# Performance work log

Measured on AMD Instinct MI355X. Metric: run time of the kernel, lower is better.

The kernel has to match this reference:

```python
import jax, jax.numpy as jnp
import numpy as np

EPS = 1e-5  # BatchNorm2d default eps


def _binarize_ste(x):
    """Forward: sign(x). Backward: hardtanh STE (grad 1 where |x|<=1, else 0)."""
    xc = jnp.clip(x, -1.0, 1.0)
    return xc + jax.lax.stop_gradient(jnp.sign(x) - xc)


def setup_inputs() -> dict:
    key = jax.random.key(0)
    k1, k2, k3, k4 = jax.random.split(key, 4)
    x = jax.random.normal(k1, (32, 256, 32, 32), dtype=jnp.float32)
    # BatchNorm affine params (affine=True)
    gamma = 1.0 + 0.1 * jax.random.normal(k2, (256,), dtype=jnp.float32)
    beta = 0.1 * jax.random.normal(k3, (256,), dtype=jnp.float32)
    # Conv weight, OIHW, bias=False
    W = 0.05 * jax.random.normal(k4, (256, 256, 3, 3), dtype=jnp.float32)
    return {"x": x, "gamma": gamma, "beta": beta, "W": W}


def reference(x, gamma, beta, W):
    # BatchNorm2d, training-mode batch statistics over (N, H, W) per channel
    mean = jnp.mean(x, axis=(0, 2, 3), keepdims=True)
    var = jnp.var(x, axis=(0, 2, 3), keepdims=True)
    xn = (x - mean) * jax.lax.rsqrt(var + EPS)
    xn = xn * gamma[None, :, None, None] + beta[None, :, None, None]
    # Conv2d_1w1a: binarize activations and weights (sign fwd / STE bwd), then conv
    a = _binarize_ste(xn)
    wb = _binarize_ste(W)
    out = jax.lax.conv_general_dilated(
        a, wb,
        window_strides=(1, 1),
        padding=((1, 1), (1, 1)),
        dimension_numbers=("NCHW", "OIHW", "NCHW"),
    )
    return out
```

## Files before the change

kernel.cpp:

```cpp
#include <hip/hip_runtime.h>
#include <hip/hip_bf16.h>


#define NIMG 32
#define C    256
#define K    256

typedef int v4i  __attribute__((ext_vector_type(4)));
typedef int v16i __attribute__((ext_vector_type(16)));

#define AHT_IMG 295936
#define AHT_KB  36992
#define AHT_ROW 1088

#define GL16(gp, lp) __builtin_amdgcn_global_load_lds(                        \
    (const __attribute__((address_space(1))) unsigned int*)(gp),              \
    (__attribute__((address_space(3))) unsigned int*)(lp), 16, 0, 0)


__global__ __launch_bounds__(256) void k_stats_packw(
    const float* __restrict__ x, const float* __restrict__ W,
    double2* __restrict__ partials, char* __restrict__ wfrag) {
  int bx = blockIdx.x;
  int tid = threadIdx.x;
  if (bx >= 2048) {
    int k = bx - 2048, c = tid;
    const float* src = W + ((size_t)k * 256 + c) * 9;
    char* dst = wfrag + (size_t)(c >> 4) * 4096 + k * 16 + (c & 15);
    #pragma unroll
    for (int t = 0; t < 9; ++t)
      dst[(size_t)t * 65536] = (src[t] > 0.0f) ? (char)1 : (char)-1;
    return;
  }
  int c = bx >> 3, grp = bx & 7;
  double s = 0.0, sq = 0.0;
  #pragma unroll
  for (int ni = 0; ni < 4; ++ni) {
    int n = grp * 4 + ni;
    const float* p = x + (size_t)n * (C * 1024) + (size_t)c * 1024;
    float4 v = ((const float4*)p)[tid];
    s += (double)v.x + (double)v.y + (double)v.z + (double)v.w;
    sq += (double)v.x * v.x + (double)v.y * v.y
        + (double)v.z * v.z + (double)v.w * v.w;
  }
  for (int o = 32; o > 0; o >>= 1) {
    s += __shfl_down(s, o);
    sq += __shfl_down(sq, o);
  }
  __shared__ double ls[4], lq[4];
  if ((tid & 63) == 0) { ls[tid >> 6] = s; lq[tid >> 6] = sq; }
  __syncthreads();
  if (tid == 0) {
    double2 r;
    r.x = ls[0] + ls[1] + ls[2] + ls[3];
    r.y = lq[0] + lq[1] + lq[2] + lq[3];
    partials[c * 8 + grp] = r;
  }
}

__global__ __launch_bounds__(256) void k_packa_i8(
    const float* __restrict__ x, const double2* __restrict__ partials,
    const float* __restrict__ gamma, const float* __restrict__ beta,
    char* __restrict__ aHT) {
  __shared__ float lf[32 * 257];
  __shared__ float lthr[256];
  __shared__ unsigned lfl[256];
  int y = blockIdx.x, n = blockIdx.y, tid = threadIdx.x;

  {
    double S = 0.0, Q = 0.0;
    #pragma unroll
    for (int g = 0; g < 8; ++g) {
      double2 p = partials[tid * 8 + g];
      S += p.x; Q += p.y;
    }
    const double N = 32768.0;
    double mean = S / N;
    double var = Q / N - mean * mean;
    double rs = 1.0 / sqrt(var + 1e-5);
    double gm = (double)gamma[tid];
    double bt = (double)beta[tid];
    float t;
    unsigned flip;
    if (gm == 0.0) {
      t = (bt > 0.0) ? -3.0e38f : 3.0e38f;
      flip = 0u;
    } else {
      t = (float)(mean - bt / (rs * gm));
      flip = (gm < 0.0) ? 1u : 0u;
    }
    lthr[tid] = t;
    lfl[tid] = flip;
  }

  #pragma unroll
  for (int it = 0; it < 8; ++it) {
    int c = it * 32 + (tid >> 3), q = tid & 7;
    float4 v = *(const float4*)(x + (size_t)n * 262144 + (size_t)c * 1024
                                + y * 32 + q * 4);
    lf[(q * 4 + 0) * 257 + c] = v.x;
    lf[(q * 4 + 1) * 257 + c] = v.y;
    lf[(q * 4 + 2) * 257 + c] = v.z;
    lf[(q * 4 + 3) * 257 + c] = v.w;
  }
  __syncthreads();
  int xl = tid & 31, cb = tid >> 5;
  unsigned wds[8];
  #pragma unroll
  for (int g = 0; g < 8; ++g) {
    unsigned wv = 0;
    #pragma unroll
    for (int jj = 0; jj < 4; ++jj) {
      int c = cb * 32 + g * 4 + jj;
      float v = lf[xl * 257 + c];
      unsigned bit = ((v > lthr[c]) ? 1u : 0u) ^ lfl[c];
      unsigned byte = bit ? 0x01u : 0xFFu;
      wv |= byte << (8 * jj);
    }
    wds[g] = wv;
  }
  char* dst = aHT + ((size_t)n * 8 + cb) * AHT_KB
            + (size_t)(y + 1) * AHT_ROW + (size_t)(xl + 1) * 32;
  uint4 u0, u1;
  u0.x = wds[0]; u0.y = wds[1]; u0.z = wds[2]; u0.w = wds[3];
  u1.x = wds[4]; u1.y = wds[5]; u1.z = wds[6]; u1.w = wds[7];
  *(uint4*)dst = u0;
  *((uint4*)dst + 1) = u1;

  uint4 z; z.x = 0; z.y = 0; z.z = 0; z.w = 0;
  if (xl < 2) {
    char* hz = aHT + ((size_t)n * 8 + cb) * AHT_KB
             + (size_t)(y + 1) * AHT_ROW + (size_t)(xl * 33) * 32;
    *(uint4*)hz = z;
    *((uint4*)hz + 1) = z;
  }
  if (y == 0 || y == 31) {
    int row = (y == 0) ? 0 : 33;
    for (int idx = tid; idx < 272; idx += 256) {
      int kb = idx / 34, xx = idx % 34;
      char* hz = aHT + ((size_t)n * 8 + kb) * AHT_KB
               + (size_t)row * AHT_ROW + (size_t)xx * 32;
      *(uint4*)hz = z;
      *((uint4*)hz + 1) = z;
    }
  }
}

__global__ __launch_bounds__(512) void k_conv_mfma(
    const char* __restrict__ aHT, const char* __restrict__ wfrag,
    float* __restrict__ out) {
  __shared__ char As[49152];
  int tid = threadIdx.x;
  int lane = tid & 63, w = tid >> 6;
  int nh = w & 3, mb = w >> 2;
  int bx = blockIdx.x;
  int lb = (bx & 7) * 32 + (bx >> 3);
  int n = lb >> 3, ys = lb & 7;
  int y0 = ys * 4;
  int yw = y0 + mb * 2;
  int xl = lane & 31, hi = lane >> 5;

  int sr = w >> 1, skb = w & 1;
  int sp = lane & 31, sh = lane >> 5;
  const char* aLane = aHT + (size_t)n * AHT_IMG + (size_t)skb * AHT_KB
                    + (size_t)sp * 32 + sh * 16;

  unsigned aRd = (unsigned)(mb * 4096 + hi * 512 + xl * 16);
  unsigned bRd = (unsigned)(hi * 4096 + (nh * 64 + xl) * 16);

  v16i a00 = {0}, a01 = {0}, a10 = {0}, a11 = {0};

  {
    const char* ag = aLane + (size_t)(y0 + 0 + sr) * AHT_ROW + 0;
    GL16(ag, As + w * 1024);
    const char* bg = wfrag + (size_t)(2 * w) * 1024 + lane * 16;
    GL16(bg, As + 8192 + (2 * w) * 1024);
    GL16(bg + 1024, As + 8192 + (2 * w + 1) * 1024);
  }
  __syncthreads();

  for (int p = 0; p < 36; ++p) {
    int cur = (p & 1) * 24576;
    if (p < 35) {
      int nxt = 24576 - cur;
      int pp = p + 1;
      int tt = pp >> 2;
      int kb0 = (pp & 3) * 2;
      int dy = tt / 3 - 1, dx = tt % 3 - 1;
      const char* ag = aLane + (size_t)kb0 * AHT_KB
                     + (size_t)(y0 + 1 + dy + sr) * AHT_ROW
                     + (size_t)(1 + dx) * 32;
      GL16(ag, As + nxt + w * 1024);
      const char* bg = wfrag + (size_t)pp * 16384 + (size_t)(2 * w) * 1024
                     + lane * 16;
      GL16(bg, As + nxt + 8192 + (2 * w) * 1024);
      GL16(bg + 1024, As + nxt + 8192 + (2 * w + 1) * 1024);
    }
    {
      const char* cb = As + cur;
      v4i A00 = *(const v4i*)(cb + aRd);
      v4i A01 = *(const v4i*)(cb + aRd + 1024);
      v4i A10 = *(const v4i*)(cb + aRd + 2048);
      v4i A11 = *(const v4i*)(cb + aRd + 3072);
      const char* bb = cb + 8192;
      v4i B0 = *(const v4i*)(bb + bRd);
      v4i B1 = *(const v4i*)(bb + bRd + 512);
      v4i B2 = *(const v4i*)(bb + bRd + 8192);
      v4i B3 = *(const v4i*)(bb + bRd + 8192 + 512);
      a00 = __builtin_amdgcn_mfma_i32_32x32x32_i8(A00, B0, a00, 0, 0, 0);
      a01 = __builtin_amdgcn_mfma_i32_32x32x32_i8(A00, B1, a01, 0, 0, 0);
      a10 = __builtin_amdgcn_mfma_i32_32x32x32_i8(A10, B0, a10, 0, 0, 0);
      a11 = __builtin_amdgcn_mfma_i32_32x32x32_i8(A10, B1, a11, 0, 0, 0);
      a00 = __builtin_amdgcn_mfma_i32_32x32x32_i8(A01, B2, a00, 0, 0, 0);
      a01 = __builtin_amdgcn_mfma_i32_32x32x32_i8(A01, B3, a01, 0, 0, 0);
      a10 = __builtin_amdgcn_mfma_i32_32x32x32_i8(A11, B2, a10, 0, 0, 0);
      a11 = __builtin_amdgcn_mfma_i32_32x32x32_i8(A11, B3, a11, 0, 0, 0);
    }
    __syncthreads();
  }

  size_t ob0 = (size_t)n * 262144 + (size_t)(nh * 64 + xl) * 1024
             + (size_t)yw * 32 + 4 * hi;
  #pragma unroll
  for (int r = 0; r < 2; ++r) {
    #pragma unroll
    for (int nb = 0; nb < 2; ++nb) {
      v16i av = (r == 0) ? (nb == 0 ? a00 : a01) : (nb == 0 ? a10 : a11);
      float* obp = out + ob0 + (size_t)nb * 32768 + r * 32;
      #pragma unroll
      for (int q = 0; q < 4; ++q) {
        float4 f;
        f.x = (float)av[q * 4 + 0];
        f.y = (float)av[q * 4 + 1];
        f.z = (float)av[q * 4 + 2];
        f.w = (float)av[q * 4 + 3];
        *(float4*)(obp + 8 * q) = f;
      }
    }
  }
}


__global__ __launch_bounds__(256) void k_stats_part_fb(
    const float* __restrict__ x, double2* __restrict__ partials) {
  int grp = blockIdx.x;
  int c = blockIdx.y;
  int tid = threadIdx.x;
  double s = 0.0, sq = 0.0;
  #pragma unroll
  for (int ni = 0; ni < 4; ++ni) {
    int n = grp * 4 + ni;
    const float* p = x + (size_t)n * (C * 1024) + (size_t)c * 1024;
    float4 v = ((const float4*)p)[tid];
    s += (double)v.x + (double)v.y + (double)v.z + (double)v.w;
    sq += (double)v.x * v.x + (double)v.y * v.y
        + (double)v.z * v.z + (double)v.w * v.w;
  }
  for (int o = 32; o > 0; o >>= 1) {
    s += __shfl_down(s, o);
    sq += __shfl_down(sq, o);
  }
  __shared__ double ls[4], lq[4];
  if ((tid & 63) == 0) { ls[tid >> 6] = s; lq[tid >> 6] = sq; }
  __syncthreads();
  if (tid == 0) {
    double2 r;
    r.x = ls[0] + ls[1] + ls[2] + ls[3];
    r.y = lq[0] + lq[1] + lq[2] + lq[3];
    partials[c * 8 + grp] = r;
  }
}

__global__ __launch_bounds__(256) void k_packw_corr_final(
    const float* __restrict__ W, const double2* __restrict__ partials,
    const float* __restrict__ gamma, const float* __restrict__ beta,
    unsigned* __restrict__ wp, int* __restrict__ corr,
    unsigned* __restrict__ zp, float* __restrict__ t_out,
    unsigned* __restrict__ flip_out) {
  int bk = blockIdx.x;
  int tid = threadIdx.x;
  if (bk == 256) {
    int c = tid;
    double S = 0.0, Q = 0.0;
    #pragma unroll
    for (int g = 0; g < 8; ++g) {
      double2 p = partials[c * 8 + g];
      S += p.x; Q += p.y;
    }
    const double N = 32768.0;
    double mean = S / N;
    double var = Q / N - mean * mean;
    double rs = 1.0 / sqrt(var + 1e-5);
    double g = (double)gamma[c];
    double b = (double)beta[c];
    float t;
    unsigned flip;
    if (g == 0.0) {
      t = (b > 0.0) ? -3.0e38f : 3.0e38f;
      flip = 0u;
    } else {
      t = (float)(mean - b / (rs * g));
      flip = (g < 0.0) ? 1u : 0u;
    }
    t_out[c] = t;
    flip_out[c] = flip;
    return;
  }
  int k = bk;
  __shared__ unsigned lw[72];
  float w[9];
  const float* src = W + (size_t)k * 2304 + (size_t)tid * 9;
  #pragma unroll
  for (int t = 0; t < 9; ++t) w[t] = src[t];
  int lane = tid & 63, wv = tid >> 6;
  #pragma unroll
  for (int t = 0; t < 9; ++t) {
    unsigned long long m = __ballot(w[t] > 0.0f);
    if (lane == 0) {
      lw[t * 8 + 2 * wv] = (unsigned)m;
      lw[t * 8 + 2 * wv + 1] = (unsigned)(m >> 32);
    }
  }
  __syncthreads();
  if (tid < 72) wp[(size_t)k * 72 + tid] = lw[tid];
  if (tid >= 128 && tid < 144) {
    int cls = tid - 128;
    int sum = 0;
    #pragma unroll
    for (int t = 0; t < 9; ++t) {
      int dy = t / 3 - 1, dx = t % 3 - 1;
      bool inv = (((cls & 1) && dx == -1) || ((cls & 2) && dx == 1) ||
                  ((cls & 4) && dy == -1) || ((cls & 8) && dy == 1));
      if (inv) {
        #pragma unroll
        for (int j = 0; j < 8; ++j) sum += __popc(lw[t * 8 + j]);
      }
    }
    corr[k * 16 + cls] = sum;
  }
  if (bk == 0 && tid >= 192 && tid < 200) zp[tid - 192] = 0u;
}

__global__ __launch_bounds__(256) void k_packa_bits(
    const float* __restrict__ x, const float* __restrict__ t,
    const unsigned* __restrict__ flip, unsigned* __restrict__ ap) {
  int n = blockIdx.y;
  int p0 = blockIdx.x * 64;
  int pix = threadIdx.x & 63;
  int q = threadIdx.x >> 6;
  unsigned w0 = 0, w1 = 0;
  const float* xb = x + (size_t)n * (C * 1024) + p0 + pix;
  #pragma unroll
  for (int i = 0; i < 64; ++i) {
    int c = q * 64 + i;
    float tv = t[c];
    unsigned fl = flip[c];
    float v = xb[(size_t)c * 1024];
    unsigned bit = ((v > tv) ? 1u : 0u) ^ fl;
    if (i < 32) w0 |= bit << i;
    else        w1 |= bit << (i - 32);
  }
  uint2 st; st.x = w0; st.y = w1;
  *(uint2*)(ap + ((size_t)n * 1024 + p0 + pix) * 8 + q * 2) = st;
}

__global__ __launch_bounds__(256) void k_conv_pop(
    const unsigned* __restrict__ ap, const unsigned* __restrict__ wp,
    const int* __restrict__ corr, const unsigned* __restrict__ zp,
    float* __restrict__ out) {
  int n = blockIdx.z;
  int ystrip = blockIdx.y;
  int kc = blockIdx.x;
  int tid = threadIdx.x;
  int lane = tid & 63;
  int wave = tid >> 6;
  int y = ystrip * 8 + wave * 2 + (lane >> 5);
  int xx = lane & 31;
  int cls = (xx == 0 ? 1 : 0) | (xx == 31 ? 2 : 0) |
            (y == 0 ? 4 : 0) | (y == 31 ? 8 : 0);
  uint4 a0[9], a1[9];
  int nv = 0;
  const uint4* zp4 = (const uint4*)zp;
  #pragma unroll
  for (int t = 0; t < 9; ++t) {
    int dy = t / 3 - 1, dx = t % 3 - 1;
    int cy = y + dy, cx = xx + dx;
    bool valid = (cy >= 0) & (cy < 32) & (cx >= 0) & (cx < 32);
    nv += valid ? 1 : 0;
    const uint4* pa = valid
        ? (const uint4*)(ap + (((size_t)n * 32 + cy) * 32 + cx) * 8)
        : zp4;
    a0[t] = pa[0];
    a1[t] = pa[1];
  }
  int bias = nv << 8;
  float* ob = out + (size_t)n * (K * 1024) + (size_t)y * 32 + xx;
  for (int kk = 0; kk < 16; ++kk) {
    int k = kc * 16 + kk;
    const uint4* wq = (const uint4*)(wp + (size_t)k * 72);
    int s0 = 0, s1 = 0, s2 = 0, s3 = 0, s4 = 0, s5 = 0, s6 = 0, s7 = 0;
    #pragma unroll
    for (int t = 0; t < 9; ++t) {
      uint4 wa = wq[t * 2];
      uint4 wb = wq[t * 2 + 1];
      s0 += __popc(a0[t].x ^ wa.x);
      s1 += __popc(a0[t].y ^ wa.y);
      s2 += __popc(a0[t].z ^ wa.z);
      s3 += __popc(a0[t].w ^ wa.w);
      s4 += __popc(a1[t].x ^ wb.x);
      s5 += __popc(a1[t].y ^ wb.y);
      s6 += __popc(a1[t].z ^ wb.z);
      s7 += __popc(a1[t].w ^ wb.w);
    }
    int S = ((s0 + s1) + (s2 + s3)) + ((s4 + s5) + (s6 + s7));
    int tot = corr[(k << 4) + cls] - S;
    ob[(size_t)k * 1024] = (float)(bias + 2 * tot);
  }
}


extern "C" void kernel_launch(void* const* d_in, const int* in_sizes, int n_in,
                              void* d_out, int out_size, void* d_ws, size_t ws_size,
                              hipStream_t stream) {
  const float* x = (const float*)d_in[0];
  const float* gamma = (const float*)d_in[1];
  const float* beta = (const float*)d_in[2];
  const float* W = (const float*)d_in[3];
  float* out = (float*)d_out;
  char* ws = (char*)d_ws;

  const size_t NEED = 655360 + (size_t)NIMG * AHT_IMG;
  if (ws_size >= NEED) {
    double2* partials = (double2*)(ws + 4096);
    char* wfrag = ws + 36864;
    char* aHT = ws + 655360;

    k_stats_packw<<<2304, 256, 0, stream>>>(x, W, partials, wfrag);
    k_packa_i8<<<dim3(32, 32), 256, 0, stream>>>(x, partials, gamma, beta, aHT);
    k_conv_mfma<<<256, 512, 0, stream>>>(aHT, wfrag, out);
  } else {
    float* t = (float*)ws;
    unsigned* flip = (unsigned*)(ws + 1024);
    unsigned* wp = (unsigned*)(ws + 4096);
    unsigned* zp = (unsigned*)(ws + 77824);
    int* corr = (int*)(ws + 78336);
    double2* partials = (double2*)(ws + 98304);
    unsigned* ap = (unsigned*)(ws + 131072);

    k_stats_part_fb<<<dim3(8, 256), 256, 0, stream>>>(x, partials);
    k_packw_corr_final<<<257, 256, 0, stream>>>(W, partials, gamma, beta,
                                                wp, corr, zp, t, flip);
    k_packa_bits<<<dim3(16, 32), 256, 0, stream>>>(x, t, flip, ap);
    k_conv_pop<<<dim3(16, 4, 32), 256, 0, stream>>>(ap, wp, corr, zp, out);
  }
}
```

Before: 53.98 us.

## Triple-buffer conv LDS stages with prefetch depth two and one barrier

The conv kernel moves from double to triple LDS buffering. Loads for stage p+2 are issued while stage p is computed, using explicit vmcnt waits and a single s_barrier per iteration in place of two __syncthreads. The goal is to hide more global-to-LDS latency and cut synchronisation per step. LDS use per block grows from 48KB to 72KB, which can lower how many blocks fit on a CU.

```diff
diff --git a/kernel.cpp b/kernel.cpp
--- a/kernel.cpp
+++ b/kernel.cpp
@@ -149,7 +149,7 @@
 __global__ __launch_bounds__(512) void k_conv_mfma(
     const char* __restrict__ aHT, const char* __restrict__ wfrag,
     float* __restrict__ out) {
-  __shared__ char As[49152];
+  __shared__ char As[73728];
   int tid = threadIdx.x;
   int lane = tid & 63, w = tid >> 6;
   int nh = w & 3, mb = w >> 2;
@@ -164,49 +164,51 @@
   int sp = lane & 31, sh = lane >> 5;
   const char* aLane = aHT + (size_t)n * AHT_IMG + (size_t)skb * AHT_KB
                     + (size_t)sp * 32 + sh * 16;
+  const char* bLane = wfrag + (size_t)(2 * w) * 1024 + lane * 16;
+  unsigned aDstW = (unsigned)(w * 1024);
+  unsigned bDstW = (unsigned)(8192 + (2 * w) * 1024);
 
   unsigned aRd = (unsigned)(mb * 4096 + hi * 512 + xl * 16);
-  unsigned bRd = (unsigned)(hi * 4096 + (nh * 64 + xl) * 16);
+  unsigned bRd = (unsigned)(8192 + hi * 4096 + (nh * 64 + xl) * 16);
 
   v16i a00 = {0}, a01 = {0}, a10 = {0}, a11 = {0};
 
-  {
-    const char* ag = aLane + (size_t)(y0 + 0 + sr) * AHT_ROW + 0;
-    GL16(ag, As + w * 1024);
-    const char* bg = wfrag + (size_t)(2 * w) * 1024 + lane * 16;
-    GL16(bg, As + 8192 + (2 * w) * 1024);
-    GL16(bg + 1024, As + 8192 + (2 * w + 1) * 1024);
-  }
-  __syncthreads();
-
+  #define ISSUE_STAGE(s, bufo)                                                \
+    {                                                                         \
+      int tt_ = (s) >> 2, kb0_ = ((s) & 3) * 2;                               \
+      int dy_ = tt_ / 3 - 1, dx_ = tt_ % 3 - 1;                               \
+      const char* ag_ = aLane + (size_t)kb0_ * AHT_KB                         \
+                      + (size_t)(y0 + 1 + dy_ + sr) * AHT_ROW                 \
+                      + (size_t)(1 + dx_) * 32;                               \
+      GL16(ag_, As + (bufo) + aDstW);                                         \
+      const char* bg_ = bLane + (size_t)(s) * 16384;                          \
+      GL16(bg_, As + (bufo) + bDstW);                                         \
+      GL16(bg_ + 1024, As + (bufo) + bDstW + 1024);                           \
+    }
+
+  ISSUE_STAGE(0, 0u);
+  ISSUE_STAGE(1, 24576u);
+
+  unsigned o0 = 0u, o1 = 24576u, o2 = 49152u;
   for (int p = 0; p < 36; ++p) {
-    int cur = (p & 1) * 24576;
     if (p < 35) {
-      int nxt = 24576 - cur;
-      int pp = p + 1;
-      int tt = pp >> 2;
-      int kb0 = (pp & 3) * 2;
-      int dy = tt / 3 - 1, dx = tt % 3 - 1;
-      const char* ag = aLane + (size_t)kb0 * AHT_KB
-                     + (size_t)(y0 + 1 + dy + sr) * AHT_ROW
-                     + (size_t)(1 + dx) * 32;
-      GL16(ag, As + nxt + w * 1024);
-      const char* bg = wfrag + (size_t)pp * 16384 + (size_t)(2 * w) * 1024
-                     + lane * 16;
-      GL16(bg, As + nxt + 8192 + (2 * w) * 1024);
-      GL16(bg + 1024, As + nxt + 8192 + (2 * w + 1) * 1024);
-    }
+      asm volatile("s_waitcnt vmcnt(3)" ::: "memory");
+    } else {
+      asm volatile("s_waitcnt vmcnt(0)" ::: "memory");
+    }
+    __builtin_amdgcn_s_barrier();
+    __builtin_amdgcn_sched_barrier(0);
+    if (p < 34) ISSUE_STAGE(p + 2, o2);
     {
-      const char* cb = As + cur;
+      const char* cb = As + o0;
       v4i A00 = *(const v4i*)(cb + aRd);
       v4i A01 = *(const v4i*)(cb + aRd + 1024);
       v4i A10 = *(const v4i*)(cb + aRd + 2048);
       v4i A11 = *(const v4i*)(cb + aRd + 3072);
-      const char* bb = cb + 8192;
-      v4i B0 = *(const v4i*)(bb + bRd);
-      v4i B1 = *(const v4i*)(bb + bRd + 512);
-      v4i B2 = *(const v4i*)(bb + bRd + 8192);
-      v4i B3 = *(const v4i*)(bb + bRd + 8192 + 512);
+      v4i B0 = *(const v4i*)(cb + bRd);
+      v4i B1 = *(const v4i*)(cb + bRd + 512);
+      v4i B2 = *(const v4i*)(cb + bRd + 8192);
+      v4i B3 = *(const v4i*)(cb + bRd + 8192 + 512);
       a00 = __builtin_amdgcn_mfma_i32_32x32x32_i8(A00, B0, a00, 0, 0, 0);
       a01 = __builtin_amdgcn_mfma_i32_32x32x32_i8(A00, B1, a01, 0, 0, 0);
       a10 = __builtin_amdgcn_mfma_i32_32x32x32_i8(A10, B0, a10, 0, 0, 0);
@@ -216,8 +218,9 @@
       a10 = __builtin_amdgcn_mfma_i32_32x32x32_i8(A11, B2, a10, 0, 0, 0);
       a11 = __builtin_amdgcn_mfma_i32_32x32x32_i8(A11, B3, a11, 0, 0, 0);
     }
-    __syncthreads();
-  }
+    unsigned t_ = o0; o0 = o1; o1 = o2; o2 = t_;
+  }
+  #undef ISSUE_STAGE
 
   size_t ob0 = (size_t)n * 262144 + (size_t)(nh * 64 + xl) * 1024
              + (size_t)yw * 32 + 4 * hi;
```

New measurement: 49.68 us. 8.0% less time.
